# Optimization experiments

Measured on AMD Instinct MI355X. Metric: run time of the kernel, lower is better.

The kernel has to match this reference:

```python
import jax, jax.numpy as jnp
import numpy as np

B, H, S, D = 2, 16, 2048, 64
MASK_NEG = 1e9


def setup_inputs() -> dict:
    key = jax.random.key(0)
    kq, kk, kv, km = jax.random.split(key, 4)
    Q = jax.random.normal(kq, (B, H, S, D), dtype=jnp.float32)
    K = jax.random.normal(kk, (B, H, S, D), dtype=jnp.float32)
    V = jax.random.normal(kv, (B, H, S, D), dtype=jnp.float32)
    # float 0/1 mask, broadcast over heads; 1 = masked-out position
    attn_mask = jax.random.randint(km, (B, 1, S, S), 0, 2).astype(jnp.float32)
    return {"Q": Q, "K": K, "V": V, "attn_mask": attn_mask}


def reference(Q, K, V, attn_mask):
    # scores: [B, H, S, S]
    attn_score = jnp.einsum('bhqd,bhkd->bhqk', Q, K)
    scale = jnp.sqrt(jnp.asarray(K.shape[-1], dtype=jnp.float32))
    attn_scale = attn_score / scale - MASK_NEG * attn_mask
    attn_prob = jax.nn.softmax(attn_scale, axis=-1)
    attn_out = jnp.einsum('bhqk,bhkd->bhqd', attn_prob, V)
    return attn_out
```

## Files before the change

kernel.cpp:

```cpp
#include <hip/hip_runtime.h>


#define S_LEN 2048
#define D_DIM 64
#define WPR   32
#define NIT   32

typedef __attribute__((ext_vector_type(8)))  short bf16x8;
typedef __attribute__((ext_vector_type(4)))  float f32x4;
typedef __attribute__((ext_vector_type(16))) float f32x16;
typedef unsigned uint2v __attribute__((ext_vector_type(2)));
typedef unsigned long long ull;

__device__ __forceinline__ f32x16 mfma32(bf16x8 a, bf16x8 b, f32x16 c) {
  return __builtin_amdgcn_mfma_f32_32x32x16_bf16(a, b, c, 0, 0, 0);
}
__device__ __forceinline__ f32x4 mfma16(bf16x8 a, bf16x8 b, f32x4 c) {
  return __builtin_amdgcn_mfma_f32_16x16x32_bf16(a, b, c, 0, 0, 0);
}
__device__ __forceinline__ unsigned short f2bf(float f) {
  unsigned u = __builtin_bit_cast(unsigned, f);
  unsigned r = u + 0x7FFFu + ((u >> 16) & 1u);
  return (unsigned short)(r >> 16);
}
__device__ __forceinline__ float bf2f(unsigned short s) {
  unsigned u = ((unsigned)s) << 16;
  return __builtin_bit_cast(float, u);
}
__device__ __forceinline__ unsigned packbf(float a, float b) {
  unsigned r;
  asm("v_cvt_pk_bf16_f32 %0, %1, %2" : "=v"(r) : "v"(a), "v"(b));
  return r;
}
__device__ __forceinline__ float fexp2(float x) {
#if __has_builtin(__builtin_amdgcn_exp2f)
  return __builtin_amdgcn_exp2f(x);
#else
  return exp2f(x);
#endif
}
__device__ __forceinline__ bool detect_bf16(const void* maskp) {
  const unsigned short* s = (const unsigned short*)maskp;
  unsigned short v = s[2 * (threadIdx.x & 63)];
  return __ballot(v == (unsigned short)0x3F80) != 0ull;
}
__device__ __forceinline__ int4 cvt_f8(const float* p) {
  float4 f0 = *(const float4*)p;
  float4 f1 = *(const float4*)(p + 4);
  int4 r;
  r.x = (int)packbf(f0.x, f0.y);
  r.y = (int)packbf(f0.z, f0.w);
  r.z = (int)packbf(f1.x, f1.y);
  r.w = (int)packbf(f1.z, f1.w);
  return r;
}
__device__ __forceinline__ void gl_lds16(const unsigned short* g, unsigned short* l) {
#if __has_builtin(__builtin_amdgcn_global_load_lds)
  __builtin_amdgcn_global_load_lds(
      (const __attribute__((address_space(1))) unsigned int*)g,
      (__attribute__((address_space(3))) unsigned int*)l, 16, 0, 0);
#else
  *(int4*)((char*)l + (threadIdx.x & 63) * 16) = *(const int4*)g;
#endif
}

#define C1 0.18033688011112042f
#define C2 1.4426950408889634e9f

#define SEG0 4096u
#define SEG1 2048u
#define SEG2 1024u
#define SEG3 2048u

__global__ __launch_bounds__(256) void prep_all(
    const void* __restrict__ M, const void* __restrict__ Kin,
    const void* __restrict__ Vin, const void* __restrict__ Qin,
    ull* __restrict__ bits, unsigned short* __restrict__ Kf,
    unsigned short* __restrict__ Vf, unsigned short* __restrict__ Qc) {
  __shared__ __align__(16) unsigned short T[64 * 72];
  const bool isb = detect_bf16(M);
  const unsigned bx = blockIdx.x;
  const int tid = threadIdx.x;

  if (bx < SEG0) {
    unsigned e0 = bx * 2048u + tid;
    #pragma unroll
    for (int j = 0; j < 8; ++j) {
      unsigned idx = e0 + (unsigned)j * 256u;
      bool on = isb ? (bf2f(((const unsigned short*)M)[idx]) > 0.5f)
                    : (((const float*)M)[idx] > 0.5f);
      ull bm = __ballot(on);
      if ((tid & 63) == 0) {
        unsigned c = idx & 2047u, r = (idx >> 11) & 2047u, bb = idx >> 22;
        bits[(((size_t)(bb * WPR + (c >> 6))) << 11) + r] = bm;
      }
    }
  } else if (bx < SEG0 + SEG1) {
    if (isb) return;
    unsigned g = (bx - SEG0) * 256u + tid;
    unsigned lane = g & 63u, f = (g >> 6) & 7u, it = (g >> 9) & 31u, bh = g >> 14;
    unsigned t = f >> 2, dc = f & 3, hi = lane >> 5, l31 = lane & 31;
    size_t src = (size_t)bh * (S_LEN * D_DIM) +
                 (size_t)(it * 64 + t * 32 + l31) * D_DIM + dc * 16 + hi * 8;
    *(int4*)&Kf[(size_t)g * 8] = cvt_f8((const float*)Kin + src);
  } else if (bx < SEG0 + SEG1 + SEG2) {
    unsigned idx = bx - (SEG0 + SEG1);
    unsigned bh = idx >> 5, it = idx & 31u;
    {
      int k = tid >> 2, d0 = (tid & 3) * 16;
      size_t src = (size_t)bh * (S_LEN * D_DIM) + (size_t)(it * 64 + k) * D_DIM + d0;
      int4 a, c;
      if (isb) {
        const unsigned short* s = (const unsigned short*)Vin + src;
        a = *(const int4*)s; c = *(const int4*)(s + 8);
      } else {
        const float* s = (const float*)Vin + src;
        a = cvt_f8(s); c = cvt_f8(s + 8);
      }
      *(int4*)&T[k * 72 + d0] = a;
      *(int4*)&T[k * 72 + d0 + 8] = c;
    }
    __syncthreads();
    #pragma unroll
    for (int h = 0; h < 2; ++h) {
      int c = tid + h * 256;
      int lane = c & 63, f = c >> 6;
      int t = f >> 2, kc = (f >> 1) & 1, dt = f & 1;
      int hi = lane >> 5, l31 = lane & 31;
      unsigned short v[8];
      #pragma unroll
      for (int j = 0; j < 8; ++j)
        v[j] = T[(t * 32 + kc * 16 + hi * 8 + j) * 72 + dt * 32 + l31];
      *(int4*)&Vf[(((size_t)(bh * 32 + it)) * 8 + f) * 512 + lane * 8] = *(int4*)v;
    }
  } else {
    if (isb) return;
    size_t i0 = ((size_t)(bx - (SEG0 + SEG1 + SEG2)) * 256 + tid) * 8;
    unsigned short v[8];
    const float* f = (const float*)Qin + i0;
    #pragma unroll
    for (int j = 0; j < 4; ++j)
      *((unsigned*)v + j) = packbf(f[2 * j] * C1, f[2 * j + 1] * C1);
    *(int4*)&Qc[i0] = *(int4*)v;
  }
}

__global__ __launch_bounds__(256) void prep_w(ull* __restrict__ bits) {
  const int tid = threadIdx.x;
  const int wave = tid >> 6;
  const int lane = tid & 63;
  const int hi = lane >> 5;
  const unsigned uid = blockIdx.x * 4 + wave;
  const unsigned b = uid >> 11, w = (uid >> 6) & 31u, q32 = uid & 63u;
  ull* base = bits + (((size_t)(b * 32 + w)) << 11) + (size_t)q32 * 32;
  const ull wc = base[lane & 31];
  #pragma unroll
  for (int sub = 0; sub < 2; ++sub) {
    #pragma unroll
    for (int r = 0; r < 16; ++r) {
      int pos = sub * 32 + (r & 3) + 8 * (r >> 2) + 4 * hi;
      ull W = __ballot(((wc >> pos) & 1ull) != 0ull);
      if (lane == 0) base[sub * 16 + r] = W;
    }
  }
}

__global__ __launch_bounds__(256, 4) void attn_fast(
    const unsigned short* __restrict__ Qc, const void* __restrict__ Qraw,
    const unsigned short* __restrict__ Kf, const void* __restrict__ Kraw,
    const unsigned short* __restrict__ Vf, const ull* __restrict__ Wm,
    const void* __restrict__ maskp, void* __restrict__ Op) {
  __shared__ __align__(16) unsigned short Stg[2][2][8][512];

  const bool isb = detect_bf16(maskp);
  const int tid  = threadIdx.x;
  const int wave = tid >> 6;
  const int lane = tid & 63;
  const int hi   = lane >> 5;
  const int l31  = lane & 31;
  const int wvu  = __builtin_amdgcn_readfirstlane(wave);
  const int g    = wvu >> 1;
  const int rw   = wvu & 1;
  const int id   = blockIdx.x;
  const int slot = id >> 3;
  const int bh   = (id & 7) * 4 + (slot & 3);
  const int qb   = slot >> 2;
  const int qbase = qb * 64 + rw * 32;
  const int b    = bh >> 4;
  const size_t base = (size_t)bh * S_LEN * D_DIM;
  const int xidx = ((lane ^ 32) & 63) * 4;

  bf16x8 qf[4];
  if (isb) {
    #pragma unroll
    for (int dc = 0; dc < 4; ++dc) {
      bf16x8 q = *(const bf16x8*)((const unsigned short*)Qraw + base +
                    (size_t)(qbase + l31) * D_DIM + dc * 16 + hi * 8);
      #pragma unroll
      for (int j = 0; j < 8; ++j)
        q[j] = (short)f2bf(bf2f((unsigned short)q[j]) * C1);
      qf[dc] = q;
    }
  } else {
    #pragma unroll
    for (int dc = 0; dc < 4; ++dc)
      qf[dc] = *(const bf16x8*)&Qc[base + (size_t)(qbase + l31) * D_DIM + dc * 16 + hi * 8];
  }

  bf16x8 onesb;
  #pragma unroll
  for (int i = 0; i < 8; ++i) onesb[i] = (short)0x3F80;

  const unsigned short* Kw0;
  size_t kd;
  if (isb) {
    Kw0 = (const unsigned short*)Kraw + base + (size_t)l31 * D_DIM + (2 * rw) * 16 + hi * 8;
    kd = 16;
  } else {
    Kw0 = Kf + (size_t)bh * 131072 + (size_t)(2 * rw) * 512 + lane * 8;
    kd = 512;
  }
  const unsigned short* Vw = Vf + (size_t)bh * 131072 + (size_t)(2 * rw) * 512 + lane * 8;
  const int ks0 = g * 32;

  const ull* WmU = Wm + (((size_t)(b * 32)) << 11) + (size_t)(qb * 2 + rw) * 32;

  f32x16 acc_o[2];
  f32x16 acc_l;
  f32x16 zv;
  #pragma unroll
  for (int r = 0; r < 16; ++r) {
    acc_o[0][r] = 0.f; acc_o[1][r] = 0.f; acc_l[r] = 0.f; zv[r] = 0.f;
  }

  {
    const size_t so = (size_t)ks0 * 2048;
    gl_lds16(Kw0 + so,      &Stg[g][0][2 * rw][0]);
    gl_lds16(Kw0 + so + kd, &Stg[g][0][2 * rw + 1][0]);
    gl_lds16(Vw + so,       &Stg[g][0][4 + 2 * rw][0]);
    gl_lds16(Vw + so + 512, &Stg[g][0][4 + 2 * rw + 1][0]);
  }
  __syncthreads();

  #pragma unroll 2
  for (int f = 0; f < 32; ++f) {
    const int cur = f & 1;
    if (f < 31) {
      const size_t so = (size_t)(ks0 + f + 1) * 2048;
      gl_lds16(Kw0 + so,      &Stg[g][cur ^ 1][2 * rw][0]);
      gl_lds16(Kw0 + so + kd, &Stg[g][cur ^ 1][2 * rw + 1][0]);
      gl_lds16(Vw + so,       &Stg[g][cur ^ 1][4 + 2 * rw][0]);
      gl_lds16(Vw + so + 512, &Stg[g][cur ^ 1][4 + 2 * rw + 1][0]);
    }
    const int ks = ks0 + f;
    const ull* Wp = WmU + (((size_t)(ks >> 1)) << 11) + (size_t)(ks & 1) * 16;

    bf16x8 ka[4];
    #pragma unroll
    for (int dc = 0; dc < 4; ++dc)
      ka[dc] = *(const bf16x8*)&Stg[g][cur][dc][lane * 8];
    __builtin_amdgcn_s_setprio(1);
    f32x16 sc = mfma32(ka[0], qf[0], zv);
    #pragma unroll
    for (int dc = 1; dc < 4; ++dc) sc = mfma32(ka[dc], qf[dc], sc);
    __builtin_amdgcn_s_setprio(0);

    float p[16];
    #pragma unroll
    for (int r = 0; r < 16; ++r) {
      float e = fexp2(sc[r]);
      ull mr = Wp[r];
      asm("v_cndmask_b32 %0, %1, 0, %2" : "=v"(p[r]) : "v"(e), "s"(mr));
    }

    #pragma unroll
    for (int kc = 0; kc < 2; ++kc) {
      unsigned pk0 = packbf(p[8 * kc + 0], p[8 * kc + 1]);
      unsigned pk1 = packbf(p[8 * kc + 2], p[8 * kc + 3]);
      unsigned pk2 = packbf(p[8 * kc + 4], p[8 * kc + 5]);
      unsigned pk3 = packbf(p[8 * kc + 6], p[8 * kc + 7]);
      uint4 d;
#if __has_builtin(__builtin_amdgcn_permlane32_swap)
      uint2v s02 = __builtin_amdgcn_permlane32_swap(pk0, pk2, false, false);
      uint2v s13 = __builtin_amdgcn_permlane32_swap(pk1, pk3, false, false);
      d.x = s02[0]; d.z = s02[1];
      d.y = s13[0]; d.w = s13[1];
#else
      unsigned x0 = (unsigned)__builtin_amdgcn_ds_bpermute(xidx, (int)pk0);
      unsigned x1 = (unsigned)__builtin_amdgcn_ds_bpermute(xidx, (int)pk1);
      unsigned x2 = (unsigned)__builtin_amdgcn_ds_bpermute(xidx, (int)pk2);
      unsigned x3 = (unsigned)__builtin_amdgcn_ds_bpermute(xidx, (int)pk3);
      d.x = hi ? x2 : pk0;
      d.y = hi ? x3 : pk1;
      d.z = hi ? pk2 : x0;
      d.w = hi ? pk3 : x1;
#endif
      bf16x8 pf = __builtin_bit_cast(bf16x8, d);
      __builtin_amdgcn_s_setprio(1);
      #pragma unroll
      for (int dt = 0; dt < 2; ++dt) {
        bf16x8 vfr = *(const bf16x8*)&Stg[g][cur][4 + kc * 2 + dt][lane * 8];
        acc_o[dt] = mfma32(pf, vfr, acc_o[dt]);
      }
      acc_l = mfma32(pf, onesb, acc_l);
      __builtin_amdgcn_s_setprio(0);
    }

    __syncthreads();
  }

  float* Cb = (float*)Stg;
  if (g == 1) {
    #pragma unroll
    for (int r = 0; r < 16; ++r) {
      Cb[(rw * 48 + r) * 64 + lane]      = acc_o[0][r];
      Cb[(rw * 48 + 16 + r) * 64 + lane] = acc_o[1][r];
      Cb[(rw * 48 + 32 + r) * 64 + lane] = acc_l[r];
    }
  }
  __syncthreads();
  if (g == 0) {
    #pragma unroll
    for (int r = 0; r < 16; ++r) {
      float o0 = acc_o[0][r] + Cb[(rw * 48 + r) * 64 + lane];
      float o1 = acc_o[1][r] + Cb[(rw * 48 + 16 + r) * 64 + lane];
      float lv = acc_l[r]    + Cb[(rw * 48 + 32 + r) * 64 + lane];
      int m = (r & 3) + 8 * (r >> 2) + 4 * hi;
      float inv = 1.0f / lv;
      size_t idx = base + (size_t)(qbase + m) * D_DIM + l31;
      if (isb) {
        ((unsigned short*)Op)[idx]      = f2bf(o0 * inv);
        ((unsigned short*)Op)[idx + 32] = f2bf(o1 * inv);
      } else {
        ((float*)Op)[idx]      = o0 * inv;
        ((float*)Op)[idx + 32] = o1 * inv;
      }
    }
  }
}

__global__ __launch_bounds__(256, 2) void attn_fallback(
    const void* __restrict__ Qp, const void* __restrict__ Kp,
    const void* __restrict__ Vp, const void* __restrict__ maskp,
    void* __restrict__ Op) {
  __shared__ __align__(16) short QKlds[128 * 72];
  __shared__ __align__(16) short Vtlds[64 * 72];
  __shared__ __align__(16) short Plds2[128 * 72];

  const bool isb = detect_bf16(maskp);
  const int tid  = threadIdx.x;
  const int wave = tid >> 6;
  const int lane = tid & 63;
  const int l15  = lane & 15;
  const int quad = lane >> 4;
  const int q0   = blockIdx.x * 128;
  const int bh   = blockIdx.y;
  const int b    = bh >> 4;
  const size_t base = (size_t)bh * S_LEN * D_DIM;

  const short* Qs = (const short*)Qp; const float* Qf = (const float*)Qp;
  const short* Ks = (const short*)Kp; const float* Kf2 = (const float*)Kp;
  const short* Vs = (const short*)Vp; const float* Vf2 = (const float*)Vp;

  if (isb) {
    const short* Qg = Qs + base + (size_t)q0 * D_DIM;
    #pragma unroll
    for (int p = 0; p < 4; ++p) {
      int e = p * 2048 + tid * 8;
      *(int4*)&QKlds[(e >> 6) * 72 + (e & 63)] = *(const int4*)(Qg + e);
    }
  } else {
    const float* Qg = Qf + base + (size_t)q0 * D_DIM;
    #pragma unroll
    for (int p = 0; p < 4; ++p) {
      int e = p * 2048 + tid * 8;
      *(int4*)&QKlds[(e >> 6) * 72 + (e & 63)] = cvt_f8(Qg + e);
    }
  }
  __syncthreads();
  bf16x8 qf[2][2];
  #pragma unroll
  for (int mi = 0; mi < 2; ++mi)
    #pragma unroll
    for (int kt = 0; kt < 2; ++kt)
      qf[mi][kt] = *(const bf16x8*)&QKlds[(wave * 32 + mi * 16 + l15) * 72 + kt * 32 + quad * 8];
  __syncthreads();

  f32x4 acc_o[2][4];
  f32x4 acc_l[2];
  const f32x4 zero4 = {0.f, 0.f, 0.f, 0.f};
  #pragma unroll
  for (int mi = 0; mi < 2; ++mi) {
    acc_l[mi] = zero4;
    #pragma unroll
    for (int nt = 0; nt < 4; ++nt) acc_o[mi][nt] = zero4;
  }
  bf16x8 onesB;
  {
    short ov = (l15 == 0) ? (short)0x3F80 : (short)0;
    #pragma unroll
    for (int i = 0; i < 8; ++i) onesB[i] = ov;
  }

  for (int it = 0; it < NIT; ++it) {
    const int k0 = it * 64;
    if (isb) {
      const short* Kg = Ks + base + (size_t)k0 * D_DIM;
      #pragma unroll
      for (int p = 0; p < 2; ++p) {
        int e = p * 2048 + tid * 8;
        *(int4*)&QKlds[(e >> 6) * 72 + (e & 63)] = *(const int4*)(Kg + e);
      }
    } else {
      const float* Kg = Kf2 + base + (size_t)k0 * D_DIM;
      #pragma unroll
      for (int p = 0; p < 2; ++p) {
        int e = p * 2048 + tid * 8;
        *(int4*)&QKlds[(e >> 6) * 72 + (e & 63)] = cvt_f8(Kg + e);
      }
    }
    {
      const int r0 = (tid >> 3) * 2;
      const int d0 = (tid & 7) * 8;
      unsigned short as_[8], bs_[8];
      if (isb) {
        const short* Vg = Vs + base + (size_t)k0 * D_DIM;
        *(int4*)as_ = *(const int4*)(Vg + r0 * D_DIM + d0);
        *(int4*)bs_ = *(const int4*)(Vg + (r0 + 1) * D_DIM + d0);
      } else {
        const float* Vg = Vf2 + base + (size_t)k0 * D_DIM;
        *(int4*)as_ = cvt_f8(Vg + r0 * D_DIM + d0);
        *(int4*)bs_ = cvt_f8(Vg + (r0 + 1) * D_DIM + d0);
      }
      #pragma unroll
      for (int j = 0; j < 8; ++j) {
        int d = d0 + j;
        int blk = (r0 >> 3) ^ (d >> 3);
        unsigned pk = (unsigned)as_[j] | ((unsigned)bs_[j] << 16);
        *(unsigned*)&Vtlds[d * 72 + blk * 8 + (r0 & 7)] = pk;
      }
    }
    __syncthreads();

    f32x4 sc[2][4];
    #pragma unroll
    for (int mi = 0; mi < 2; ++mi)
      #pragma unroll
      for (int nt = 0; nt < 4; ++nt) sc[mi][nt] = zero4;
    #pragma unroll
    for (int nt = 0; nt < 4; ++nt) {
      bf16x8 kf0 = *(const bf16x8*)&QKlds[(nt * 16 + l15) * 72 + quad * 8];
      bf16x8 kf1 = *(const bf16x8*)&QKlds[(nt * 16 + l15) * 72 + 32 + quad * 8];
      #pragma unroll
      for (int mi = 0; mi < 2; ++mi) {
        sc[mi][nt] = mfma16(qf[mi][0], kf0, sc[mi][nt]);
        sc[mi][nt] = mfma16(qf[mi][1], kf1, sc[mi][nt]);
      }
    }

    #pragma unroll
    for (int mi = 0; mi < 2; ++mi) {
      #pragma unroll
      for (int nt = 0; nt < 4; ++nt) {
        #pragma unroll
        for (int reg = 0; reg < 4; ++reg) {
          int rg = q0 + wave * 32 + mi * 16 + quad * 4 + reg;
          size_t mix = (size_t)b * S_LEN * S_LEN + (size_t)rg * S_LEN + k0 + nt * 16 + l15;
          float mv = isb ? bf2f(((const unsigned short*)maskp)[mix])
                         : ((const float*)maskp)[mix];
          float y = sc[mi][nt][reg] * C1 - mv * C2;
          Plds2[(wave * 32 + mi * 16 + quad * 4 + reg) * 72 + nt * 16 + l15] =
              (short)f2bf(fexp2(y));
        }
      }
    }
    __syncthreads();

    #pragma unroll
    for (int kt = 0; kt < 2; ++kt) {
      bf16x8 pf[2];
      #pragma unroll
      for (int mi = 0; mi < 2; ++mi)
        pf[mi] = *(const bf16x8*)&Plds2[(wave * 32 + mi * 16 + l15) * 72 + kt * 32 + quad * 8];
      #pragma unroll
      for (int nt = 0; nt < 4; ++nt) {
        int d = nt * 16 + l15;
        int kb = (kt * 4 + quad) ^ (d >> 3);
        bf16x8 vf = *(const bf16x8*)&Vtlds[d * 72 + kb * 8];
        #pragma unroll
        for (int mi = 0; mi < 2; ++mi)
          acc_o[mi][nt] = mfma16(pf[mi], vf, acc_o[mi][nt]);
      }
      #pragma unroll
      for (int mi = 0; mi < 2; ++mi)
        acc_l[mi] = mfma16(pf[mi], onesB, acc_l[mi]);
    }
    __syncthreads();
  }

  #pragma unroll
  for (int mi = 0; mi < 2; ++mi) {
    #pragma unroll
    for (int reg = 0; reg < 4; ++reg) {
      float lv = __shfl(acc_l[mi][reg], lane & 48, 64);
      float inv = 1.0f / lv;
      #pragma unroll
      for (int nt = 0; nt < 4; ++nt) {
        float o = acc_o[mi][nt][reg] * inv;
        size_t idx = base + (size_t)(q0 + wave * 32 + mi * 16 + quad * 4 + reg) * D_DIM + nt * 16 + l15;
        if (isb) ((unsigned short*)Op)[idx] = f2bf(o);
        else     ((float*)Op)[idx] = o;
      }
    }
  }
}

extern "C" void kernel_launch(void* const* d_in, const int* in_sizes, int n_in,
                              void* d_out, int out_size, void* d_ws, size_t ws_size,
                              hipStream_t stream) {
  const void* Q = d_in[0];
  const void* K = d_in[1];
  const void* V = d_in[2];
  const void* M = d_in[3];

  dim3 block(256);
  const size_t bits_bytes = (size_t)2 * S_LEN * S_LEN / 8;
  const size_t tens_bytes = (size_t)2 * 16 * S_LEN * D_DIM * 2;

  if (ws_size >= bits_bytes + 3 * tens_bytes) {
    char* ws = (char*)d_ws;
    ull* bits = (ull*)ws;
    unsigned short* Kf = (unsigned short*)(ws + bits_bytes);
    unsigned short* Vf = (unsigned short*)(ws + bits_bytes + tens_bytes);
    unsigned short* Qc = (unsigned short*)(ws + bits_bytes + 2 * tens_bytes);
    prep_all<<<dim3(SEG0 + SEG1 + SEG2 + SEG3), block, 0, stream>>>(
        M, K, V, Q, bits, Kf, Vf, Qc);
    prep_w<<<dim3(1024), block, 0, stream>>>(bits);
    attn_fast<<<dim3(1024), block, 0, stream>>>(Qc, Q, Kf, K, Vf, bits, M, d_out);
  } else {
    attn_fallback<<<dim3(S_LEN / 128, 32), block, 0, stream>>>(Q, K, V, M, d_out);
  }
}
```

Measured before the change: 170.9 us.

## Load V fragments directly to registers and split QK MFMA chain

V tiles are no longer staged through LDS. Each wave now loads its V fragments straight from global memory into registers at the start of every iteration, and the LDS staging buffer shrinks to hold only K (the combine buffer is sized separately). The QK^T MFMA chain is split into two independent accumulators that are summed before exp, which shortens the dependency chain. The trade-off is that V global loads now sit on the critical path of each iteration instead of being prefetched one step ahead, and every wave in a group redundantly loads all four V fragments.

```diff
diff --git a/kernel.cpp b/kernel.cpp
--- a/kernel.cpp
+++ b/kernel.cpp
@@ -170,7 +170,9 @@
     const unsigned short* __restrict__ Kf, const void* __restrict__ Kraw,
     const unsigned short* __restrict__ Vf, const ull* __restrict__ Wm,
     const void* __restrict__ maskp, void* __restrict__ Op) {
-  __shared__ __align__(16) unsigned short Stg[2][2][8][512];
+  __shared__ __align__(16) char ShMem[24576];
+  typedef unsigned short StgT[2][4][512];
+  StgT* Stg = (StgT*)ShMem;
 
   const bool isb = detect_bf16(maskp);
   const int tid  = threadIdx.x;
@@ -220,7 +222,7 @@
     Kw0 = Kf + (size_t)bh * 131072 + (size_t)(2 * rw) * 512 + lane * 8;
     kd = 512;
   }
-  const unsigned short* Vw = Vf + (size_t)bh * 131072 + (size_t)(2 * rw) * 512 + lane * 8;
+  const unsigned short* Vb = Vf + (size_t)bh * 131072 + lane * 8;
   const int ks0 = g * 32;
 
   const ull* WmU = Wm + (((size_t)(b * 32)) << 11) + (size_t)(qb * 2 + rw) * 32;
@@ -237,22 +239,25 @@
     const size_t so = (size_t)ks0 * 2048;
     gl_lds16(Kw0 + so,      &Stg[g][0][2 * rw][0]);
     gl_lds16(Kw0 + so + kd, &Stg[g][0][2 * rw + 1][0]);
-    gl_lds16(Vw + so,       &Stg[g][0][4 + 2 * rw][0]);
-    gl_lds16(Vw + so + 512, &Stg[g][0][4 + 2 * rw + 1][0]);
   }
   __syncthreads();
 
   #pragma unroll 2
   for (int f = 0; f < 32; ++f) {
     const int cur = f & 1;
+    const int ks = ks0 + f;
+    bf16x8 vv[4];
+    {
+      const unsigned short* Vp_ = Vb + (size_t)ks * 2048;
+      #pragma unroll
+      for (int fi = 0; fi < 4; ++fi)
+        vv[fi] = *(const bf16x8*)(Vp_ + (size_t)fi * 512);
+    }
     if (f < 31) {
-      const size_t so = (size_t)(ks0 + f + 1) * 2048;
+      const size_t so = (size_t)(ks + 1) * 2048;
       gl_lds16(Kw0 + so,      &Stg[g][cur ^ 1][2 * rw][0]);
       gl_lds16(Kw0 + so + kd, &Stg[g][cur ^ 1][2 * rw + 1][0]);
-      gl_lds16(Vw + so,       &Stg[g][cur ^ 1][4 + 2 * rw][0]);
-      gl_lds16(Vw + so + 512, &Stg[g][cur ^ 1][4 + 2 * rw + 1][0]);
-    }
-    const int ks = ks0 + f;
+    }
     const ull* Wp = WmU + (((size_t)(ks >> 1)) << 11) + (size_t)(ks & 1) * 16;
 
     bf16x8 ka[4];
@@ -260,15 +265,16 @@
     for (int dc = 0; dc < 4; ++dc)
       ka[dc] = *(const bf16x8*)&Stg[g][cur][dc][lane * 8];
     __builtin_amdgcn_s_setprio(1);
-    f32x16 sc = mfma32(ka[0], qf[0], zv);
-    #pragma unroll
-    for (int dc = 1; dc < 4; ++dc) sc = mfma32(ka[dc], qf[dc], sc);
+    f32x16 sc0 = mfma32(ka[0], qf[0], zv);
+    f32x16 sc1 = mfma32(ka[2], qf[2], zv);
+    sc0 = mfma32(ka[1], qf[1], sc0);
+    sc1 = mfma32(ka[3], qf[3], sc1);
     __builtin_amdgcn_s_setprio(0);
 
     float p[16];
     #pragma unroll
     for (int r = 0; r < 16; ++r) {
-      float e = fexp2(sc[r]);
+      float e = fexp2(sc0[r] + sc1[r]);
       ull mr = Wp[r];
       asm("v_cndmask_b32 %0, %1, 0, %2" : "=v"(p[r]) : "v"(e), "s"(mr));
     }
@@ -298,10 +304,8 @@
       bf16x8 pf = __builtin_bit_cast(bf16x8, d);
       __builtin_amdgcn_s_setprio(1);
       #pragma unroll
-      for (int dt = 0; dt < 2; ++dt) {
-        bf16x8 vfr = *(const bf16x8*)&Stg[g][cur][4 + kc * 2 + dt][lane * 8];
-        acc_o[dt] = mfma32(pf, vfr, acc_o[dt]);
-      }
+      for (int dt = 0; dt < 2; ++dt)
+        acc_o[dt] = mfma32(pf, vv[kc * 2 + dt], acc_o[dt]);
       acc_l = mfma32(pf, onesb, acc_l);
       __builtin_amdgcn_s_setprio(0);
     }
@@ -309,7 +313,7 @@
     __syncthreads();
   }
 
-  float* Cb = (float*)Stg;
+  float* Cb = (float*)ShMem;
   if (g == 1) {
     #pragma unroll
     for (int r = 0; r < 16; ++r) {
```

After: 211.8 us. 1.24x slower.
